# Kernel tuning notes

Measured on AMD Instinct MI355X. Metric: run time of the kernel, lower is better.

## Reference

```python
import jax, jax.numpy as jnp
import numpy as np

N_NODES = 50000
N_EDGES = 800000
N_LABELS = 50      # len(deplabel2idx) == len(deplabels)
EMB = 64           # dep_emb_size
HID = 96           # dep_hidden_dim


def _glorot(key, shape):
    fan_in, fan_out = shape
    lim = jnp.sqrt(6.0 / (fan_in + fan_out)).astype(jnp.float32)
    return jax.random.uniform(key, shape, jnp.float32, -lim, lim)


def setup_inputs() -> dict:
    key = jax.random.key(0)
    ks = jax.random.split(key, 10)
    dep_labels = jax.random.randint(ks[0], (N_NODES,), 0, N_LABELS)
    src = jax.random.randint(ks[1], (N_EDGES,), 0, N_NODES)
    dst = jax.random.randint(ks[2], (N_EDGES,), 0, N_NODES)
    emb = jax.random.normal(ks[3], (N_LABELS, EMB), jnp.float32)
    W1 = _glorot(ks[4], (EMB, HID)); b1 = jnp.zeros((HID,), jnp.float32)
    W2 = _glorot(ks[5], (HID, HID)); b2 = jnp.zeros((HID,), jnp.float32)
    W3 = _glorot(ks[6], (HID, N_LABELS)); b3 = jnp.zeros((N_LABELS,), jnp.float32)
    return {"dep_labels": dep_labels, "src": src, "dst": dst, "emb": emb,
            "W1": W1, "b1": b1, "W2": W2, "b2": b2, "W3": W3, "b3": b3}


def _graph_conv(h, src, dst, out_norm, in_norm, W, b, relu):
    # DGL GraphConv norm='both': D_out^{-1/2} scaling at src, sum-aggregate
    # over incoming edges, D_in^{-1/2} scaling at dst, then linear (+ act).
    m = (h * out_norm[:, None])[src]                      # [E, d]
    agg = jax.ops.segment_sum(m, dst, num_segments=h.shape[0])
    agg = agg * in_norm[:, None]                          # [N, d]
    out = agg @ W + b
    return jax.nn.relu(out) if relu else out


def reference(dep_labels, src, dst, emb, W1, b1, W2, b2, W3, b3):
    n = emb.shape[1] * 0 + N_NODES
    ones = jnp.ones((src.shape[0],), jnp.float32)
    out_deg = jax.ops.segment_sum(ones, src, num_segments=N_NODES)
    in_deg = jax.ops.segment_sum(ones, dst, num_segments=N_NODES)
    out_norm = jax.lax.rsqrt(jnp.maximum(out_deg, 1.0))
    in_norm = jax.lax.rsqrt(jnp.maximum(in_deg, 1.0))
    h = emb[dep_labels]                                   # embedding lookup [N, EMB]
    # dropout p=0.0 between layers -> identity (eval-mode reference)
    h = _graph_conv(h, src, dst, out_norm, in_norm, W1, b1, relu=True)
    h = _graph_conv(h, src, dst, out_norm, in_norm, W2, b2, relu=True)
    h = _graph_conv(h, src, dst, out_norm, in_norm, W3, b3, relu=False)
    return h
```

## Files before the change

kernel.cpp:

```cpp
#include <hip/hip_runtime.h>
#include <hip/hip_fp16.h>

#define N_NODES 50000
#define N_EDGES 800000
#define EMB     64
#define HID     96
#define NLAB    50
#define TSTRIDE 64
#define TC      13
#define NBP     256
#define EPB     ((N_EDGES + NBP - 1) / NBP)
#define NBUCK   196
#define WSTRIDE 104
#define WPREP_N (160 * WSTRIDE)
#define WPREPB  ((WPREP_N + 255) / 256)
#define T1TSTR  72
#define T1T_N   (HID * T1TSTR)
#define T1TB    ((T1T_N + 255) / 256)
#define SSTR    64
#define NMFMA   ((N_NODES + 127) / 128)

typedef _Float16 f16x8 __attribute__((ext_vector_type(8)));
typedef float f32x4 __attribute__((ext_vector_type(4)));

__device__ __forceinline__ float2 h2f(unsigned u) {
    __half2 h = *reinterpret_cast<__half2*>(&u);
    return __half22float2(h);
}
__device__ __forceinline__ unsigned f2h(float a, float b) {
    __half2 h = __floats2half2_rn(a, b);
    return *reinterpret_cast<unsigned*>(&h);
}

__global__ void coarse_hist_kernel(const int* __restrict__ src, const int* __restrict__ dst,
                                   int* __restrict__ histd, int* __restrict__ hists,
                                   const float* __restrict__ emb, const float* __restrict__ W1,
                                   __half* __restrict__ T1t,
                                   const float* __restrict__ W2, const float* __restrict__ W3,
                                   __half* __restrict__ wprep) {
    int b = blockIdx.x, t = threadIdx.x;
    if (b < NBP) {
        __shared__ int hd[256], hs[256];
        hd[t] = 0; hs[t] = 0;
        __syncthreads();
        int hi = min(b * EPB + EPB, N_EDGES);
        for (int i = b * EPB + t; i < hi; i += 256) {
            atomicAdd(&hd[((unsigned)dst[i]) >> 8], 1);
            atomicAdd(&hs[((unsigned)src[i]) >> 8], 1);
        }
        __syncthreads();
        histd[b * 256 + t] = hd[t];
        hists[b * 256 + t] = hs[t];
    } else if (b < NBP + T1TB) {
        int i = (b - NBP) * 256 + t;
        if (i < T1T_N) {
            int j = i / T1TSTR, l = i - j * T1TSTR;
            float sum = 0.0f;
            if (l < NLAB) {
#pragma unroll
                for (int m = 0; m < EMB; ++m) sum += emb[l * EMB + m] * W1[m * HID + j];
            }
            T1t[i] = __float2half(sum);
        }
    } else {
        int i = (b - NBP - T1TB) * 256 + t;
        if (i < WPREP_N) {
            int j = i / WSTRIDE, kk = i - j * WSTRIDE;
            float v = 0.0f;
            if (kk < HID) {
                if (j < HID) v = W2[kk * HID + j];
                else { int jj = j - HID; if (jj < NLAB) v = W3[kk * NLAB + jj]; }
            }
            wprep[i] = __float2half(v);
        }
    }
}

__global__ void coarse_scan_kernel(const int* __restrict__ histd, const int* __restrict__ hists,
                                   int* __restrict__ blkrel_d, int* __restrict__ blkrel_s,
                                   int* __restrict__ bbase_d, int* __restrict__ bbase_s) {
    __shared__ int sh[256];
    int t = threadIdx.x;
    const int* hist = blockIdx.x ? hists : histd;
    int* blkrel     = blockIdx.x ? blkrel_s : blkrel_d;
    int* bbase      = blockIdx.x ? bbase_s : bbase_d;
    int run = 0;
#pragma unroll 16
    for (int b = 0; b < NBP; ++b) {
        blkrel[b * 256 + t] = run;
        run += hist[b * 256 + t];
    }
    sh[t] = run;
    __syncthreads();
    for (int off = 1; off < 256; off <<= 1) {
        int v = sh[t];
        if (t >= off) v += sh[t - off];
        __syncthreads();
        sh[t] = v;
        __syncthreads();
    }
    bbase[t] = sh[t] - run;
}

__global__ void partition_kernel(const int* __restrict__ src, const int* __restrict__ dst,
                                 const int* __restrict__ blkrel_d, const int* __restrict__ blkrel_s,
                                 const int* __restrict__ bbase_d, const int* __restrict__ bbase_s,
                                 int* __restrict__ dstp, unsigned char* __restrict__ srcp) {
    __shared__ int curd[256], curs[256];
    int b = blockIdx.x, t = threadIdx.x;
    curd[t] = bbase_d[t] + blkrel_d[b * 256 + t];
    curs[t] = bbase_s[t] + blkrel_s[b * 256 + t];
    __syncthreads();
    int hi = min(b * EPB + EPB, N_EDGES);
    for (int i = b * EPB + t; i < hi; i += 256) {
        int d = dst[i], s = src[i];
        int pd = atomicAdd(&curd[((unsigned)d) >> 8], 1);
        dstp[pd] = s | ((d & 0xFF) << 16);
        int ps = atomicAdd(&curs[((unsigned)s) >> 8], 1);
        srcp[ps] = (unsigned char)(s & 0xFF);
    }
}

__global__ void fine_hist_kernel(const int* __restrict__ dstp, const unsigned char* __restrict__ srcp,
                                 const int* __restrict__ bbase_d, const int* __restrict__ bbase_s,
                                 const int* __restrict__ labels,
                                 int* __restrict__ deg_in, int* __restrict__ deg_out,
                                 float* __restrict__ out_norm, int2* __restrict__ node_info,
                                 int* __restrict__ bsum) {
    __shared__ int cnt[256];
    int b = blockIdx.x, t = threadIdx.x;
    cnt[t] = 0;
    __syncthreads();
    if (b < NBUCK) {
        int lo = bbase_d[b], hi = bbase_d[b + 1];
        for (int i = lo + t; i < hi; i += 256)
            atomicAdd(&cnt[(dstp[i] >> 16) & 0xFF], 1);
        __syncthreads();
        int node = b * 256 + t;
        if (node < N_NODES) deg_in[node] = cnt[t];
        for (int off = 128; off > 0; off >>= 1) {
            __syncthreads();
            if (t < off) cnt[t] += cnt[t + off];
        }
        if (t == 0) bsum[b] = cnt[0];
    } else {
        int bb = b - NBUCK;
        int lo = bbase_s[bb], hi = bbase_s[bb + 1];
        for (int i = lo + t; i < hi; i += 256)
            atomicAdd(&cnt[srcp[i]], 1);
        __syncthreads();
        int node = bb * 256 + t;
        if (node < N_NODES) {
            int d = cnt[t];
            deg_out[node] = d;
            float on = rsqrtf(fmaxf((float)d, 1.0f));
            out_norm[node] = on;
            node_info[node] = make_int2(labels[node] << 16, __float_as_int(on));
        }
    }
}

__global__ void scan_scatter_kernel(const int* __restrict__ deg_in, const int* __restrict__ bsum,
                                    const int* __restrict__ dstp, const int* __restrict__ bbase_d,
                                    const int2* __restrict__ node_info,
                                    int* __restrict__ row_off, float* __restrict__ in_norm,
                                    unsigned short* __restrict__ esrc, float* __restrict__ S) {
    __shared__ int pb[256];
    __shared__ int s[256];
    __shared__ int ro[256];
    __shared__ int cur[256];
    __shared__ float Sl[256][NLAB];
    int t = threadIdx.x, b = blockIdx.x, i = b * 256 + t;
    for (int idx = t; idx < 256 * NLAB; idx += 256) ((float*)Sl)[idx] = 0.0f;
    pb[t] = (t < b) ? bsum[t] : 0;
    int own = (i < N_NODES) ? deg_in[i] : 0;
    s[t] = own;
    cur[t] = 0;
    __syncthreads();
    for (int off = 128; off > 0; off >>= 1) {
        if (t < off) pb[t] += pb[t + off];
        __syncthreads();
    }
    int base = pb[0];
    for (int off = 1; off < 256; off <<= 1) {
        int v = s[t];
        if (t >= off) v += s[t - off];
        __syncthreads();
        s[t] = v;
        __syncthreads();
    }
    int r0 = base + s[t] - own;
    ro[t] = r0;
    if (i < N_NODES) {
        row_off[i] = r0;
        in_norm[i] = rsqrtf(fmaxf((float)own, 1.0f));
    }
    __syncthreads();
    int lo = bbase_d[b], hi = bbase_d[b + 1];
    for (int k = lo + t; k < hi; k += 256) {
        int rec = dstp[k];
        int sn = rec & 0xFFFF;
        int nl = (rec >> 16) & 0xFF;
        int r = atomicAdd(&cur[nl], 1);
        esrc[ro[nl] + r] = (unsigned short)sn;
        int2 ni = node_info[sn];
        atomicAdd(&Sl[nl][((unsigned)ni.x) >> 16], __int_as_float(ni.y));
    }
    __syncthreads();
    for (int idx = t; idx < 256 * SSTR; idx += 256) {
        int n = idx >> 6, c = idx & 63;
        int node = b * 256 + n;
        if (node < N_NODES)
            S[(size_t)node * SSTR + c] = (c < NLAB) ? Sl[n][c] : 0.0f;
    }
}

__global__ __launch_bounds__(512) void h1_mfma_kernel(
        const float* __restrict__ S, const __half* __restrict__ T1t,
        const float* __restrict__ b1, const float* __restrict__ in_norm,
        const float* __restrict__ out_norm, __half* __restrict__ h1s) {
    const int tid = threadIdx.x;
    const int w = tid >> 6, l = tid & 63;
    const int lr = l & 15, lg = l >> 4;
    const int n0 = blockIdx.x * 128 + w * 16;

    f16x8 a[2];
    {
        int n = n0 + lr; if (n > N_NODES - 1) n = N_NODES - 1;
        const float* sp = S + (size_t)n * SSTR + lg * 8;
#pragma unroll
        for (int kb = 0; kb < 2; ++kb) {
            float4 v0 = *(const float4*)(sp + kb * 32);
            float4 v1 = *(const float4*)(sp + kb * 32 + 4);
            a[kb] = (f16x8){(_Float16)v0.x, (_Float16)v0.y, (_Float16)v0.z, (_Float16)v0.w,
                            (_Float16)v1.x, (_Float16)v1.y, (_Float16)v1.z, (_Float16)v1.w};
        }
    }
    f32x4 acc[6];
#pragma unroll
    for (int nt = 0; nt < 6; ++nt) {
        acc[nt] = (f32x4){0.f, 0.f, 0.f, 0.f};
#pragma unroll
        for (int kb = 0; kb < 2; ++kb) {
            f16x8 bfr = *(const f16x8*)(T1t + (nt * 16 + lr) * T1TSTR + kb * 32 + lg * 8);
            acc[nt] = __builtin_amdgcn_mfma_f32_16x16x32_f16(a[kb], bfr, acc[nt], 0, 0, 0);
        }
    }
    float on4[4], in4[4];
#pragma unroll
    for (int r = 0; r < 4; ++r) {
        int n = n0 + lg * 4 + r; if (n > N_NODES - 1) n = N_NODES - 1;
        on4[r] = out_norm[n];
        in4[r] = in_norm[n];
    }
#pragma unroll
    for (int nt = 0; nt < 6; ++nt) {
        int col = nt * 16 + lr;
        float bb = b1[col];
#pragma unroll
        for (int r = 0; r < 4; ++r) {
            int n = n0 + lg * 4 + r;
            if (n < N_NODES) {
                float v = fmaxf(in4[r] * acc[nt][r] + bb, 0.f) * on4[r];
                h1s[(size_t)n * HID + col] = __float2half(v);
            }
        }
    }
}

__global__ __launch_bounds__(512) void agg_linear23_kernel(
        const __half* __restrict__ hs, const int* __restrict__ row_off,
        const int* __restrict__ deg, const unsigned short* __restrict__ esrc,
        const float* __restrict__ in_norm, const __half* __restrict__ wprep,
        const float* __restrict__ b2, const float* __restrict__ out_norm,
        __half* __restrict__ t) {
    __shared__ _Float16 Wl[WPREP_N];
    __shared__ _Float16 A[128][WSTRIDE];
    const int tid = threadIdx.x;
    {
        const uint4* sp = (const uint4*)wprep;
        uint4* dp = (uint4*)Wl;
        for (int i = tid; i < WPREP_N / 8; i += 512) dp[i] = sp[i];
    }
    const int n0b = blockIdx.x * 128;

    for (int task = tid; task < 128 * 12; task += 512) {
        int m = task / 12;
        int c = task - m * 12;
        int n = n0b + m;
        uint2 rA = make_uint2(0u, 0u), rB = make_uint2(0u, 0u);
        if (n < N_NODES) {
            const __half* p0 = hs + c * 4;
            const __half* p1 = hs + (c + 12) * 4;
            int k = row_off[n];
            int e = k + deg[n];
            float ax = 0.f, ay = 0.f, az = 0.f, aw = 0.f;
            float bx = 0.f, by = 0.f, bz = 0.f, bw = 0.f;
            for (; k + 3 < e; k += 4) {
                size_t r0 = (size_t)esrc[k] * HID;
                size_t r1 = (size_t)esrc[k + 1] * HID;
                size_t r2 = (size_t)esrc[k + 2] * HID;
                size_t r3 = (size_t)esrc[k + 3] * HID;
                uint2 aA = *(const uint2*)(p0 + r0); uint2 bA = *(const uint2*)(p1 + r0);
                uint2 aB = *(const uint2*)(p0 + r1); uint2 bB = *(const uint2*)(p1 + r1);
                uint2 aC = *(const uint2*)(p0 + r2); uint2 bC = *(const uint2*)(p1 + r2);
                uint2 aD = *(const uint2*)(p0 + r3); uint2 bD = *(const uint2*)(p1 + r3);
                float2 f;
                f = h2f(aA.x); ax += f.x; ay += f.y;  f = h2f(aA.y); az += f.x; aw += f.y;
                f = h2f(aB.x); ax += f.x; ay += f.y;  f = h2f(aB.y); az += f.x; aw += f.y;
                f = h2f(aC.x); ax += f.x; ay += f.y;  f = h2f(aC.y); az += f.x; aw += f.y;
                f = h2f(aD.x); ax += f.x; ay += f.y;  f = h2f(aD.y); az += f.x; aw += f.y;
                f = h2f(bA.x); bx += f.x; by += f.y;  f = h2f(bA.y); bz += f.x; bw += f.y;
                f = h2f(bB.x); bx += f.x; by += f.y;  f = h2f(bB.y); bz += f.x; bw += f.y;
                f = h2f(bC.x); bx += f.x; by += f.y;  f = h2f(bC.y); bz += f.x; bw += f.y;
                f = h2f(bD.x); bx += f.x; by += f.y;  f = h2f(bD.y); bz += f.x; bw += f.y;
            }
            for (; k < e; ++k) {
                size_t r0 = (size_t)esrc[k] * HID;
                uint2 aA = *(const uint2*)(p0 + r0); uint2 bA = *(const uint2*)(p1 + r0);
                float2 f;
                f = h2f(aA.x); ax += f.x; ay += f.y;  f = h2f(aA.y); az += f.x; aw += f.y;
                f = h2f(bA.x); bx += f.x; by += f.y;  f = h2f(bA.y); bz += f.x; bw += f.y;
            }
            float nn = in_norm[n];
            rA.x = f2h(ax * nn, ay * nn); rA.y = f2h(az * nn, aw * nn);
            rB.x = f2h(bx * nn, by * nn); rB.y = f2h(bz * nn, bw * nn);
        }
        *(uint2*)(&A[m][c * 4]) = rA;
        *(uint2*)(&A[m][(c + 12) * 4]) = rB;
    }
    __syncthreads();

    const int w = tid >> 6, l = tid & 63;
    const int lr = l & 15, lg = l >> 4;
    const int m0 = w * 16;
    const int n0 = n0b + m0;

    f16x8 a[3];
#pragma unroll
    for (int kb = 0; kb < 3; ++kb)
        a[kb] = *(const f16x8*)(&A[m0 + lr][kb * 32 + lg * 8]);
    f32x4 acc[6];
#pragma unroll
    for (int nt = 0; nt < 6; ++nt) {
        acc[nt] = (f32x4){0.f, 0.f, 0.f, 0.f};
#pragma unroll
        for (int kb = 0; kb < 3; ++kb) {
            f16x8 bfr = *(const f16x8*)(&Wl[(nt * 16 + lr) * WSTRIDE + kb * 32 + lg * 8]);
            acc[nt] = __builtin_amdgcn_mfma_f32_16x16x32_f16(a[kb], bfr, acc[nt], 0, 0, 0);
        }
    }
    float on4[4];
#pragma unroll
    for (int r = 0; r < 4; ++r) {
        int n = n0 + lg * 4 + r; if (n > N_NODES - 1) n = N_NODES - 1;
        on4[r] = out_norm[n];
    }
    asm volatile("s_waitcnt lgkmcnt(0)" ::: "memory");
#pragma unroll
    for (int nt = 0; nt < 6; ++nt) {
        int col = nt * 16 + lr;
        float bb = b2[col];
#pragma unroll
        for (int r = 0; r < 4; ++r) {
            float v = fmaxf(acc[nt][r] + bb, 0.f) * on4[r];
            A[m0 + lg * 4 + r][col] = (_Float16)v;
        }
    }
    asm volatile("s_waitcnt lgkmcnt(0)" ::: "memory");

    f16x8 a2[3];
#pragma unroll
    for (int kb = 0; kb < 3; ++kb)
        a2[kb] = *(const f16x8*)(&A[m0 + lr][kb * 32 + lg * 8]);
#pragma unroll
    for (int nt = 0; nt < 4; ++nt) {
        f32x4 acc2 = (f32x4){0.f, 0.f, 0.f, 0.f};
#pragma unroll
        for (int kb = 0; kb < 3; ++kb) {
            f16x8 bfr = *(const f16x8*)(&Wl[(HID + nt * 16 + lr) * WSTRIDE + kb * 32 + lg * 8]);
            acc2 = __builtin_amdgcn_mfma_f32_16x16x32_f16(a2[kb], bfr, acc2, 0, 0, 0);
        }
        int col = nt * 16 + lr;
        if (col < 4 * TC) {
#pragma unroll
            for (int r = 0; r < 4; ++r) {
                int n = n0 + lg * 4 + r;
                if (n < N_NODES) t[(size_t)n * TSTRIDE + col] = __float2half(acc2[r]);
            }
        }
    }
}

__global__ void gather_out_kernel(const __half* __restrict__ t, const int* __restrict__ row_off,
                                  const int* __restrict__ deg, const unsigned short* __restrict__ esrc,
                                  const float* __restrict__ in_norm, const float* __restrict__ bias,
                                  float* __restrict__ out) {
    int i = blockIdx.x * blockDim.x + threadIdx.x;
    if (i >= N_NODES * TC) return;
    int n = i / TC;
    int c = i - n * TC;
    const __half* p0 = t + c * 4;
    int k = row_off[n];
    int e = k + deg[n];
    float ax = 0.f, ay = 0.f, az = 0.f, aw = 0.f;
    for (; k + 3 < e; k += 4) {
        size_t r0 = (size_t)esrc[k] * TSTRIDE;
        size_t r1 = (size_t)esrc[k + 1] * TSTRIDE;
        size_t r2 = (size_t)esrc[k + 2] * TSTRIDE;
        size_t r3 = (size_t)esrc[k + 3] * TSTRIDE;
        uint2 v0 = *(const uint2*)(p0 + r0);
        uint2 v1 = *(const uint2*)(p0 + r1);
        uint2 v2 = *(const uint2*)(p0 + r2);
        uint2 v3 = *(const uint2*)(p0 + r3);
        float2 f;
        f = h2f(v0.x); ax += f.x; ay += f.y;  f = h2f(v0.y); az += f.x; aw += f.y;
        f = h2f(v1.x); ax += f.x; ay += f.y;  f = h2f(v1.y); az += f.x; aw += f.y;
        f = h2f(v2.x); ax += f.x; ay += f.y;  f = h2f(v2.y); az += f.x; aw += f.y;
        f = h2f(v3.x); ax += f.x; ay += f.y;  f = h2f(v3.y); az += f.x; aw += f.y;
    }
    for (; k < e; ++k) {
        size_t r0 = (size_t)esrc[k] * TSTRIDE;
        uint2 v0 = *(const uint2*)(p0 + r0);
        float2 f;
        f = h2f(v0.x); ax += f.x; ay += f.y;  f = h2f(v0.y); az += f.x; aw += f.y;
    }
    float nn = in_norm[n];
    int j = c * 4;
    float* op = out + (size_t)n * NLAB + j;
    float2 lo; lo.x = ax * nn + bias[j];     lo.y = ay * nn + bias[j + 1];
    *(float2*)op = lo;
    if (j + 2 < NLAB) {
        float2 hi; hi.x = az * nn + bias[j + 2]; hi.y = aw * nn + bias[j + 3];
        *(float2*)(op + 2) = hi;
    }
}

static inline int cdiv(long a, int b) { return (int)((a + b - 1) / b); }

extern "C" void kernel_launch(void* const* d_in, const int* in_sizes, int n_in,
                              void* d_out, int out_size, void* d_ws, size_t ws_size,
                              hipStream_t stream) {
    const int*   dep_labels = (const int*)d_in[0];
    const int*   src        = (const int*)d_in[1];
    const int*   dst        = (const int*)d_in[2];
    const float* emb        = (const float*)d_in[3];
    const float* W1 = (const float*)d_in[4]; const float* b1 = (const float*)d_in[5];
    const float* W2 = (const float*)d_in[6]; const float* b2 = (const float*)d_in[7];
    const float* W3 = (const float*)d_in[8]; const float* b3 = (const float*)d_in[9];
    float* out = (float*)d_out;

    int* wsp           = (int*)d_ws;
    int* row_off       = wsp;                 wsp += N_NODES;
    int* deg_in        = wsp;                 wsp += N_NODES;
    int* deg_out_a     = wsp;                 wsp += N_NODES;
    int* bsum          = wsp;                 wsp += 256;
    float* out_norm    = (float*)wsp;         wsp += N_NODES;
    float* in_norm     = (float*)wsp;         wsp += N_NODES;
    int2* node_info    = (int2*)wsp;          wsp += 2 * N_NODES;
    __half* T1t        = (__half*)wsp;        wsp += T1T_N / 2 + 8;
    __half* wprep      = (__half*)wsp;        wsp += WPREP_N / 2;
    unsigned short* esrc = (unsigned short*)wsp; wsp += N_EDGES / 2;
    int* bufA          = wsp;                 wsp += (size_t)N_NODES * HID;
    __half* bufH       = (__half*)wsp;
    __half* tbuf  = (__half*)bufA;
    float*  Sbuf  = (float*)(bufA + 1600000);
    int* histd    = bufA;
    int* hists    = histd + NBP * 256;
    int* blkrel_d = hists + NBP * 256;
    int* blkrel_s = blkrel_d + NBP * 256;
    int* bbase_d  = blkrel_s + NBP * 256;
    int* bbase_s  = bbase_d + 256;
    int* dstp     = bbase_s + 256;
    unsigned char* srcp = (unsigned char*)(dstp + N_EDGES);

    const int B = 256;

    coarse_hist_kernel<<<NBP + T1TB + WPREPB, B, 0, stream>>>(src, dst, histd, hists,
                                                              emb, W1, T1t, W2, W3, wprep);
    coarse_scan_kernel<<<2, B, 0, stream>>>(histd, hists, blkrel_d, blkrel_s, bbase_d, bbase_s);
    partition_kernel<<<NBP, B, 0, stream>>>(src, dst, blkrel_d, blkrel_s, bbase_d, bbase_s,
                                            dstp, srcp);
    fine_hist_kernel<<<2 * NBUCK, B, 0, stream>>>(dstp, srcp, bbase_d, bbase_s, dep_labels,
                                                  deg_in, deg_out_a, out_norm, node_info, bsum);
    scan_scatter_kernel<<<NBUCK, B, 0, stream>>>(deg_in, bsum, dstp, bbase_d, node_info,
                                                 row_off, in_norm, esrc, Sbuf);

    h1_mfma_kernel<<<NMFMA, 512, 0, stream>>>(Sbuf, T1t, b1, in_norm, out_norm, bufH);

    agg_linear23_kernel<<<NMFMA, 512, 0, stream>>>(
        bufH, row_off, deg_in, esrc, in_norm, wprep, b2, out_norm, tbuf);

    gather_out_kernel<<<cdiv((long)N_NODES * TC, B), B, 0, stream>>>(
        tbuf, row_off, deg_in, esrc, in_norm, b3, out);
}
```

Before: 198.1 us.

## Fuse dst fine histogram and layer-1 MFMA into scan-scatter kernel

The in-degree histogram moves into the scan/scatter kernel, with row offsets taken from the bucket base bbase_d instead of a global block-sum scan. The layer-1 MFMA now reads the per-node label sums straight from shared memory, so the S intermediate never goes to global memory and one launch is dropped. This removes a global write and read of S plus a kernel boundary. In exchange, the MFMA work runs on 256-thread blocks with each wave handling 64 rows, and the large shared array may lower occupancy.

Result: no change. 201.8 us (+1.9%).

```diff
diff --git a/kernel.cpp b/kernel.cpp
--- a/kernel.cpp
+++ b/kernel.cpp
@@ -17,7 +17,6 @@
 #define T1TSTR  72
 #define T1T_N   (HID * T1TSTR)
 #define T1TB    ((T1T_N + 255) / 256)
-#define SSTR    64
 #define NMFMA   ((N_NODES + 127) / 128)
 
 typedef _Float16 f16x8 __attribute__((ext_vector_type(8)));
@@ -121,82 +120,66 @@
     }
 }
 
-__global__ void fine_hist_kernel(const int* __restrict__ dstp, const unsigned char* __restrict__ srcp,
-                                 const int* __restrict__ bbase_d, const int* __restrict__ bbase_s,
-                                 const int* __restrict__ labels,
-                                 int* __restrict__ deg_in, int* __restrict__ deg_out,
-                                 float* __restrict__ out_norm, int2* __restrict__ node_info,
-                                 int* __restrict__ bsum) {
+__global__ void fine_hist_src_kernel(const unsigned char* __restrict__ srcp,
+                                     const int* __restrict__ bbase_s,
+                                     const int* __restrict__ labels,
+                                     float* __restrict__ out_norm,
+                                     int2* __restrict__ node_info) {
     __shared__ int cnt[256];
     int b = blockIdx.x, t = threadIdx.x;
     cnt[t] = 0;
     __syncthreads();
-    if (b < NBUCK) {
-        int lo = bbase_d[b], hi = bbase_d[b + 1];
-        for (int i = lo + t; i < hi; i += 256)
-            atomicAdd(&cnt[(dstp[i] >> 16) & 0xFF], 1);
-        __syncthreads();
-        int node = b * 256 + t;
-        if (node < N_NODES) deg_in[node] = cnt[t];
-        for (int off = 128; off > 0; off >>= 1) {
-            __syncthreads();
-            if (t < off) cnt[t] += cnt[t + off];
-        }
-        if (t == 0) bsum[b] = cnt[0];
-    } else {
-        int bb = b - NBUCK;
-        int lo = bbase_s[bb], hi = bbase_s[bb + 1];
-        for (int i = lo + t; i < hi; i += 256)
-            atomicAdd(&cnt[srcp[i]], 1);
-        __syncthreads();
-        int node = bb * 256 + t;
-        if (node < N_NODES) {
-            int d = cnt[t];
-            deg_out[node] = d;
-            float on = rsqrtf(fmaxf((float)d, 1.0f));
-            out_norm[node] = on;
-            node_info[node] = make_int2(labels[node] << 16, __float_as_int(on));
-        }
-    }
-}
-
-__global__ void scan_scatter_kernel(const int* __restrict__ deg_in, const int* __restrict__ bsum,
-                                    const int* __restrict__ dstp, const int* __restrict__ bbase_d,
-                                    const int2* __restrict__ node_info,
-                                    int* __restrict__ row_off, float* __restrict__ in_norm,
-                                    unsigned short* __restrict__ esrc, float* __restrict__ S) {
-    __shared__ int pb[256];
-    __shared__ int s[256];
+    int lo = bbase_s[b], hi = bbase_s[b + 1];
+    for (int i = lo + t; i < hi; i += 256)
+        atomicAdd(&cnt[srcp[i]], 1);
+    __syncthreads();
+    int node = b * 256 + t;
+    if (node < N_NODES) {
+        float on = rsqrtf(fmaxf((float)cnt[t], 1.0f));
+        out_norm[node] = on;
+        node_info[node] = make_int2(labels[node] << 16, __float_as_int(on));
+    }
+}
+
+__global__ __launch_bounds__(256) void scan_scatter_h1_kernel(
+        const int* __restrict__ dstp, const int* __restrict__ bbase_d,
+        const int2* __restrict__ node_info,
+        const __half* __restrict__ T1t, const float* __restrict__ b1,
+        const float* __restrict__ out_norm,
+        int* __restrict__ deg_in, int* __restrict__ row_off, float* __restrict__ in_norm,
+        unsigned short* __restrict__ esrc, __half* __restrict__ h1s) {
+    __shared__ float Sl[256][NLAB];
+    __shared__ int cnt[256];
     __shared__ int ro[256];
     __shared__ int cur[256];
-    __shared__ float Sl[256][NLAB];
-    int t = threadIdx.x, b = blockIdx.x, i = b * 256 + t;
+    __shared__ int sc[256];
+    int t = threadIdx.x, b = blockIdx.x;
+    int node = b * 256 + t;
     for (int idx = t; idx < 256 * NLAB; idx += 256) ((float*)Sl)[idx] = 0.0f;
-    pb[t] = (t < b) ? bsum[t] : 0;
-    int own = (i < N_NODES) ? deg_in[i] : 0;
-    s[t] = own;
-    cur[t] = 0;
-    __syncthreads();
-    for (int off = 128; off > 0; off >>= 1) {
-        if (t < off) pb[t] += pb[t + off];
-        __syncthreads();
-    }
-    int base = pb[0];
+    cnt[t] = 0; cur[t] = 0;
+    __syncthreads();
+    int lo = bbase_d[b], hi = bbase_d[b + 1];
+    for (int k = lo + t; k < hi; k += 256)
+        atomicAdd(&cnt[(dstp[k] >> 16) & 0xFF], 1);
+    __syncthreads();
+    int own = cnt[t];
+    sc[t] = own;
+    __syncthreads();
     for (int off = 1; off < 256; off <<= 1) {
-        int v = s[t];
-        if (t >= off) v += s[t - off];
-        __syncthreads();
-        s[t] = v;
-        __syncthreads();
-    }
-    int r0 = base + s[t] - own;
+        int v = sc[t];
+        if (t >= off) v += sc[t - off];
+        __syncthreads();
+        sc[t] = v;
+        __syncthreads();
+    }
+    int r0 = lo + sc[t] - own;
     ro[t] = r0;
-    if (i < N_NODES) {
-        row_off[i] = r0;
-        in_norm[i] = rsqrtf(fmaxf((float)own, 1.0f));
-    }
-    __syncthreads();
-    int lo = bbase_d[b], hi = bbase_d[b + 1];
+    if (node < N_NODES) {
+        deg_in[node] = own;
+        row_off[node] = r0;
+        in_norm[node] = rsqrtf(fmaxf((float)own, 1.0f));
+    }
+    __syncthreads();
     for (int k = lo + t; k < hi; k += 256) {
         int rec = dstp[k];
         int sn = rec & 0xFFFF;
@@ -207,62 +190,39 @@
         atomicAdd(&Sl[nl][((unsigned)ni.x) >> 16], __int_as_float(ni.y));
     }
     __syncthreads();
-    for (int idx = t; idx < 256 * SSTR; idx += 256) {
-        int n = idx >> 6, c = idx & 63;
-        int node = b * 256 + n;
-        if (node < N_NODES)
-            S[(size_t)node * SSTR + c] = (c < NLAB) ? Sl[n][c] : 0.0f;
-    }
-}
-
-__global__ __launch_bounds__(512) void h1_mfma_kernel(
-        const float* __restrict__ S, const __half* __restrict__ T1t,
-        const float* __restrict__ b1, const float* __restrict__ in_norm,
-        const float* __restrict__ out_norm, __half* __restrict__ h1s) {
-    const int tid = threadIdx.x;
-    const int w = tid >> 6, l = tid & 63;
+    const int w = t >> 6, l = t & 63;
     const int lr = l & 15, lg = l >> 4;
-    const int n0 = blockIdx.x * 128 + w * 16;
-
-    f16x8 a[2];
-    {
-        int n = n0 + lr; if (n > N_NODES - 1) n = N_NODES - 1;
-        const float* sp = S + (size_t)n * SSTR + lg * 8;
+#pragma unroll
+    for (int mt = 0; mt < 4; ++mt) {
+        int mbase = w * 64 + mt * 16;
+        f16x8 a[2];
 #pragma unroll
         for (int kb = 0; kb < 2; ++kb) {
-            float4 v0 = *(const float4*)(sp + kb * 32);
-            float4 v1 = *(const float4*)(sp + kb * 32 + 4);
-            a[kb] = (f16x8){(_Float16)v0.x, (_Float16)v0.y, (_Float16)v0.z, (_Float16)v0.w,
-                            (_Float16)v1.x, (_Float16)v1.y, (_Float16)v1.z, (_Float16)v1.w};
-        }
-    }
-    f32x4 acc[6];
-#pragma unroll
-    for (int nt = 0; nt < 6; ++nt) {
-        acc[nt] = (f32x4){0.f, 0.f, 0.f, 0.f};
-#pragma unroll
-        for (int kb = 0; kb < 2; ++kb) {
-            f16x8 bfr = *(const f16x8*)(T1t + (nt * 16 + lr) * T1TSTR + kb * 32 + lg * 8);
-            acc[nt] = __builtin_amdgcn_mfma_f32_16x16x32_f16(a[kb], bfr, acc[nt], 0, 0, 0);
-        }
-    }
-    float on4[4], in4[4];
-#pragma unroll
-    for (int r = 0; r < 4; ++r) {
-        int n = n0 + lg * 4 + r; if (n > N_NODES - 1) n = N_NODES - 1;
-        on4[r] = out_norm[n];
-        in4[r] = in_norm[n];
-    }
-#pragma unroll
-    for (int nt = 0; nt < 6; ++nt) {
-        int col = nt * 16 + lr;
-        float bb = b1[col];
-#pragma unroll
-        for (int r = 0; r < 4; ++r) {
-            int n = n0 + lg * 4 + r;
-            if (n < N_NODES) {
-                float v = fmaxf(in4[r] * acc[nt][r] + bb, 0.f) * on4[r];
-                h1s[(size_t)n * HID + col] = __float2half(v);
+#pragma unroll
+            for (int i = 0; i < 8; ++i) {
+                int kk = kb * 32 + lg * 8 + i;
+                a[kb][i] = (_Float16)((kk < NLAB) ? Sl[mbase + lr][kk] : 0.0f);
+            }
+        }
+#pragma unroll
+        for (int nt = 0; nt < 6; ++nt) {
+            f32x4 acc = (f32x4){0.f, 0.f, 0.f, 0.f};
+#pragma unroll
+            for (int kb = 0; kb < 2; ++kb) {
+                f16x8 bfr = *(const f16x8*)(T1t + (nt * 16 + lr) * T1TSTR + kb * 32 + lg * 8);
+                acc = __builtin_amdgcn_mfma_f32_16x16x32_f16(a[kb], bfr, acc, 0, 0, 0);
+            }
+            int col = nt * 16 + lr;
+            float bb = b1[col];
+#pragma unroll
+            for (int r = 0; r < 4; ++r) {
+                int mrow = mbase + lg * 4 + r;
+                int n = b * 256 + mrow;
+                if (n < N_NODES) {
+                    float innv = rsqrtf(fmaxf((float)cnt[mrow], 1.0f));
+                    float v = fmaxf(innv * acc[r] + bb, 0.f) * out_norm[n];
+                    h1s[(size_t)n * HID + col] = __float2half(v);
+                }
             }
         }
     }
@@ -453,8 +413,6 @@
     int* wsp           = (int*)d_ws;
     int* row_off       = wsp;                 wsp += N_NODES;
     int* deg_in        = wsp;                 wsp += N_NODES;
-    int* deg_out_a     = wsp;                 wsp += N_NODES;
-    int* bsum          = wsp;                 wsp += 256;
     float* out_norm    = (float*)wsp;         wsp += N_NODES;
     float* in_norm     = (float*)wsp;         wsp += N_NODES;
     int2* node_info    = (int2*)wsp;          wsp += 2 * N_NODES;
@@ -464,7 +422,6 @@
     int* bufA          = wsp;                 wsp += (size_t)N_NODES * HID;
     __half* bufH       = (__half*)wsp;
     __half* tbuf  = (__half*)bufA;
-    float*  Sbuf  = (float*)(bufA + 1600000);
     int* histd    = bufA;
     int* hists    = histd + NBP * 256;
     int* blkrel_d = hists + NBP * 256;
@@ -481,12 +438,11 @@
     coarse_scan_kernel<<<2, B, 0, stream>>>(histd, hists, blkrel_d, blkrel_s, bbase_d, bbase_s);
     partition_kernel<<<NBP, B, 0, stream>>>(src, dst, blkrel_d, blkrel_s, bbase_d, bbase_s,
                                             dstp, srcp);
-    fine_hist_kernel<<<2 * NBUCK, B, 0, stream>>>(dstp, srcp, bbase_d, bbase_s, dep_labels,
-                                                  deg_in, deg_out_a, out_norm, node_info, bsum);
-    scan_scatter_kernel<<<NBUCK, B, 0, stream>>>(deg_in, bsum, dstp, bbase_d, node_info,
-                                                 row_off, in_norm, esrc, Sbuf);
-
-    h1_mfma_kernel<<<NMFMA, 512, 0, stream>>>(Sbuf, T1t, b1, in_norm, out_norm, bufH);
+    fine_hist_src_kernel<<<NBUCK, B, 0, stream>>>(srcp, bbase_s, dep_labels,
+                                                  out_norm, node_info);
+    scan_scatter_h1_kernel<<<NBUCK, B, 0, stream>>>(dstp, bbase_d, node_info, T1t, b1,
+                                                    out_norm, deg_in, row_off, in_norm,
+                                                    esrc, bufH);
 
     agg_linear23_kernel<<<NMFMA, 512, 0, stream>>>(
         bufH, row_off, deg_in, esrc, in_norm, wprep, b2, out_norm, tbuf);
```
